# Kernel tuning notes

Measured on AMD Instinct MI355X. Metric: run time of the kernel, lower is better.

The kernel has to match this reference:

```python
import jax, jax.numpy as jnp
import numpy as np

H = W = 256          # render / reference image size (module crops ref to 256x256)
TS = 4               # texture_size in the module
EYE_DIST, ELEV, AZIM = 2.732, 0.0, np.pi / 2  # fixed azimuth (orig: uniform(0,360))
EPS = 1e-8


def _look_at(verts, eye):
    # neural_renderer look_at: at=origin, up=+y
    up = jnp.array([0.0, 1.0, 0.0], dtype=verts.dtype)
    z = -eye / jnp.linalg.norm(eye)
    x = jnp.cross(up, z)
    x = x / jnp.linalg.norm(x)
    y = jnp.cross(z, x)
    R = jnp.stack([x, y, z], axis=0)  # rows = camera axes
    return (verts - eye) @ R.T


def _cross2(u, v):
    return u[..., 0] * v[..., 1] - u[..., 1] * v[..., 0]


def _render(vertices, faces, textures):
    # Orthographic (perspective=False), ambient-only lighting -> color == texture sample.
    eye = jnp.array([EYE_DIST * np.cos(ELEV) * np.sin(AZIM),
                     EYE_DIST * np.sin(ELEV),
                     -EYE_DIST * np.cos(ELEV) * np.cos(AZIM)], dtype=vertices.dtype)
    v = _look_at(vertices[0], eye)            # [V,3] camera space
    fv = v[faces[0]]                          # [F,3,3]
    a, b, c = fv[:, 0, :2], fv[:, 1, :2], fv[:, 2, :2]  # [F,2] screen-space verts
    zf = fv[..., 2]                           # [F,3] per-vertex depth

    # pixel centers in NDC, y flipped (image row 0 = top)
    xs = (jnp.arange(W, dtype=vertices.dtype) + 0.5) / W * 2.0 - 1.0
    ys = 1.0 - (jnp.arange(H, dtype=vertices.dtype) + 0.5) / H * 2.0
    P = jnp.stack(jnp.meshgrid(xs, ys, indexing='xy'), -1).reshape(-1, 2)  # [HW,2]
    Pq = P[:, None, :]                        # [HW,1,2]

    denom = _cross2(b - a, c - a)             # [F] signed 2*area
    w0 = _cross2((c - b)[None], Pq - b[None])  # [HW,F] edge functions
    w1 = _cross2((a - c)[None], Pq - c[None])
    w2 = _cross2((b - a)[None], Pq - a[None])
    s = jnp.sign(denom)[None]
    nondeg = (jnp.abs(denom) > EPS)[None]
    inside = (w0 * s >= 0) & (w1 * s >= 0) & (w2 * s >= 0) & nondeg
    d = jnp.where(jnp.abs(denom) > EPS, denom, 1.0)[None]
    w0, w1, w2 = w0 / d, w1 / d, w2 / d       # normalized barycentrics
    depth = w0 * zf[None, :, 0] + w1 * zf[None, :, 1] + w2 * zf[None, :, 2]  # [HW,F]
    visible = inside & (depth > 0)

    # z-buffer: nearest visible face per pixel
    zbuf = jnp.where(visible, depth, jnp.inf)
    best = jnp.argmin(zbuf, axis=1)           # [HW]
    hit = jnp.take_along_axis(visible, best[:, None], 1)[:, 0]
    bw = jnp.stack([jnp.take_along_axis(wi, best[:, None], 1)[:, 0]
                    for wi in (w0, w1, w2)], axis=-1)  # [HW,3]

    # sample face texture cube [TS,TS,TS] by barycentric coords (nearest)
    ti = jnp.clip(jnp.round(bw * (TS - 1)).astype(jnp.int32), 0, TS - 1)
    color = textures[0][best, ti[:, 0], ti[:, 1], ti[:, 2]]  # [HW,3]
    img = jnp.where(hit[:, None], color, jnp.zeros_like(color)).reshape(H, W, 3)
    return jnp.transpose(img, (2, 0, 1))[None]  # [1,3,H,W]


def setup_inputs() -> dict:
    key = jax.random.key(0)
    k1, k2, k3, k4 = jax.random.split(key, 4)
    V, F = 642, 512
    verts = jax.random.normal(k1, (1, V, 3), jnp.float32)
    verts = verts / (jnp.linalg.norm(verts, axis=-1, keepdims=True) + 1e-6)  # unit sphere
    faces = jax.random.randint(k2, (1, F, 3), 0, V, jnp.int32)
    textures = jax.random.normal(k3, (1, F, TS, TS, TS, 3), jnp.float32)
    image_ref = jax.random.uniform(k4, (1, 3, H, W), jnp.float32)
    return {"vertices": verts, "textures": textures, "image_ref": image_ref, "faces": faces}


def reference(vertices, textures, image_ref, faces):
    image = _render(vertices, faces, jnp.tanh(textures))
    return jnp.sum((image - image_ref) ** 2)
```

## Files before the change

### kernel.cpp

```cpp
#include <hip/hip_runtime.h>
#include <math.h>

#define NFACE 512
#define NVERT 642
#define NPIX  (256 * 256)
#define DXS   (2.0f / 256.0f)

#define EYEX 2.732f
#define EYEZ (-1.6728675276352845e-16f)
#define CC0  (6.123233995736766e-17f)

__global__ __launch_bounds__(256) void render_loss(
    const float* __restrict__ verts,
    const int*   __restrict__ faces,
    const float* __restrict__ tex,
    const float* __restrict__ ref,
    float* __restrict__ out)
{
    __shared__ float  sverts[NVERT * 3];
    __shared__ float4 sf0[NFACE];
    __shared__ float4 sf1[NFACE];
    __shared__ float4 flist[NFACE];
    __shared__ float4 pl0[NFACE];
    __shared__ float4 pl1[NFACE];
    __shared__ float2 pld[NFACE];
    __shared__ unsigned marr[4][256];
    __shared__ int   fcnt, pcnt;
    __shared__ unsigned Mu;
    __shared__ float wsum[4];

    int tid = threadIdx.x;
    if (tid == 0) { fcnt = 0; pcnt = 0; Mu = 0x7f800000u; }

    for (int k = tid; k < NVERT * 3; k += 256) sverts[k] = verts[k];
    __syncthreads();

    int tileX = (blockIdx.x & 15) << 4;
    int tileY = (blockIdx.x >> 4) << 4;
    float xlo = (tileX + 0.5f)  * DXS - 1.0f;
    float xhi = (tileX + 15.5f) * DXS - 1.0f;
    float yhi = 1.0f - (tileY + 0.5f)  * DXS;
    float ylo = 1.0f - (tileY + 15.5f) * DXS;

    float rc[2][9];
    int   rcls[2];
    float rdmn[2];
#pragma unroll
    for (int it = 0; it < 2; ++it) {
        int f = tid + it * 256;
        rcls[it] = 0;
        float vx[3], vy[3], vz[3];
#pragma unroll
        for (int k = 0; k < 3; ++k) {
            int vi = faces[f * 3 + k];
            float px = sverts[vi * 3 + 0];
            float py = sverts[vi * 3 + 1];
            float pz = sverts[vi * 3 + 2];
            float dx = px - EYEX;
            float dz = pz - EYEZ;
            vx[k] = CC0 * dx + dz;
            vy[k] = py;
            vz[k] = -dx + CC0 * dz;
        }
        float ax = vx[0], ay = vy[0];
        float bx = vx[1], by = vy[1];
        float cx = vx[2], cy = vy[2];
        float denom = (bx - ax) * (cy - ay) - (by - ay) * (cx - ax);
        if (fabsf(denom) <= 1e-8f) continue;

        float si = 1.0f / denom;
        float e0x = cx - bx, e0y = cy - by;
        float e1x = ax - cx, e1y = ay - cy;
        float e2x = bx - ax, e2y = by - ay;
        float A0 = e0x * si, B0 = -e0y * si, C0 = (e0y * bx - e0x * by) * si;
        float A1 = e1x * si, B1 = -e1y * si, C1 = (e1y * cx - e1x * cy) * si;
        float A2 = -(A0 + A1), B2 = -(B0 + B1), C2 = 1.0f - C0 - C1;
        float DA = A0 * vz[0] + A1 * vz[1] + A2 * vz[2];
        float DB = B0 * vz[0] + B1 * vz[1] + B2 * vz[2];
        float DC = C0 * vz[0] + C1 * vz[1] + C2 * vz[2];

        sf0[f] = make_float4(A0, B0, C0, A1);
        sf1[f] = make_float4(B1, C1, DA, DB);

        float bxmn = fminf(fminf(ax, bx), cx), bxmx = fmaxf(fmaxf(ax, bx), cx);
        float bymn = fminf(fminf(ay, by), cy), bymx = fmaxf(fmaxf(ay, by), cy);
        if ((bxmn > xhi + 1e-5f) | (bxmx < xlo - 1e-5f) |
            (bymn > yhi + 1e-5f) | (bymx < ylo - 1e-5f)) continue;

        float wmx[3], wmn[3], mg[3];
        float As[3] = {A0, A1, A2}, Bs[3] = {B0, B1, B2}, Cs[3] = {C0, C1, C2};
#pragma unroll
        for (int k = 0; k < 3; ++k) {
            float t1 = As[k] * ylo, t2 = As[k] * yhi;
            float u1 = Bs[k] * xlo, u2 = Bs[k] * xhi;
            wmx[k] = fmaxf(t1, t2) + fmaxf(u1, u2) + Cs[k];
            wmn[k] = fminf(t1, t2) + fminf(u1, u2) + Cs[k];
            mg[k]  = (fabsf(As[k]) + fabsf(Bs[k]) + fabsf(Cs[k])) * 2e-6f;
        }
        if ((wmx[0] < -mg[0]) | (wmx[1] < -mg[1]) | (wmx[2] < -mg[2])) continue;
        bool full = (wmn[0] > mg[0]) & (wmn[1] > mg[1]) & (wmn[2] > mg[2]);

        float t1 = DA * ylo, t2 = DA * yhi;
        float u1 = DB * xlo, u2 = DB * xhi;
        float dmx = fmaxf(t1, t2) + fmaxf(u1, u2) + DC;
        float dmn = fminf(t1, t2) + fminf(u1, u2) + DC;
        float md  = (fabsf(DA) + fabsf(DB) + fabsf(DC)) * 2e-6f + 1e-4f;
        rdmn[it] = dmn - md;
        rcls[it] = full ? 1 : 2;
        rc[it][0] = A0; rc[it][1] = B0; rc[it][2] = C0;
        rc[it][3] = A1; rc[it][4] = B1; rc[it][5] = C1;
        rc[it][6] = DA; rc[it][7] = DB; rc[it][8] = DC;
        if (full) atomicMin(&Mu, __float_as_uint(dmx + md));
    }
    __syncthreads();

    float M = __uint_as_float(Mu);
#pragma unroll
    for (int it = 0; it < 2; ++it) {
        if (rcls[it] == 0 || rdmn[it] > M) continue;
        int f = tid + it * 256;
        float fb = __uint_as_float((unsigned)f);
        if (rcls[it] == 1) {
            int s = atomicAdd(&fcnt, 1);
            flist[s] = make_float4(rc[it][6], rc[it][7], rc[it][8], fb);
        } else {
            int s = atomicAdd(&pcnt, 1);
            pl0[s] = make_float4(rc[it][0], rc[it][1], rc[it][2], rc[it][3]);
            pl1[s] = make_float4(rc[it][4], rc[it][5], rc[it][6], rc[it][7]);
            pld[s] = make_float2(rc[it][8], fb);
        }
    }
    __syncthreads();
    int fc = fcnt, pc = pcnt;

    int lane = tid & 63;
    int w    = tid >> 6;
    int col   = lane & 15;
    int rbase = (lane >> 4) << 2;
    float Px  = (tileX + col + 0.5f) * DXS - 1.0f;
    float Py0 = 1.0f - (tileY + rbase + 0.5f) * DXS;

    unsigned pk0 = 0xFFFFFFFFu, pk1 = 0xFFFFFFFFu;
    unsigned pk2 = 0xFFFFFFFFu, pk3 = 0xFFFFFFFFu;

#pragma unroll 2
    for (int k = w; k < fc; k += 4) {
        float4 r = flist[k];
        float td = fmaf(r.y, Px, r.z);
        float d0 = fmaf(r.x, Py0, td);
        float d1 = fmaf(r.x, Py0 - DXS, td);
        float d2 = fmaf(r.x, Py0 - 2.0f * DXS, td);
        float d3 = fmaf(r.x, Py0 - 3.0f * DXS, td);
        unsigned fb = __float_as_uint(r.w);
        unsigned c0 = (__float_as_uint(d0) & 0xFFFFFE00u) | fb;
        unsigned c1 = (__float_as_uint(d1) & 0xFFFFFE00u) | fb;
        unsigned c2 = (__float_as_uint(d2) & 0xFFFFFE00u) | fb;
        unsigned c3 = (__float_as_uint(d3) & 0xFFFFFE00u) | fb;
        pk0 = pk0 < c0 ? pk0 : c0;
        pk1 = pk1 < c1 ? pk1 : c1;
        pk2 = pk2 < c2 ? pk2 : c2;
        pk3 = pk3 < c3 ? pk3 : c3;
    }

#pragma unroll 2
    for (int k = w; k < pc; k += 4) {
        float4 q0 = pl0[k];
        float4 q1 = pl1[k];
        float2 qd = pld[k];
        float t0 = fmaf(q0.y, Px, q0.z);
        float t1 = fmaf(q1.x, Px, q1.y);
        float td = fmaf(q1.w, Px, qd.x);
        unsigned fb = __float_as_uint(qd.y);
#pragma unroll
        for (int q = 0; q < 4; ++q) {
            float Py = Py0 - (float)q * DXS;
            float w0 = fmaf(q0.x, Py, t0);
            float w1 = fmaf(q0.w, Py, t1);
            float w2 = 1.0f - w0 - w1;
            float dp = fmaf(q1.z, Py, td);
            float mn = fminf(fminf(w0, w1), w2);
            unsigned cd = (__float_as_uint(dp) & 0xFFFFFE00u) | fb;
            cd = (mn >= 0.f) ? cd : 0xFFFFFFFFu;
            if (q == 0) pk0 = pk0 < cd ? pk0 : cd;
            if (q == 1) pk1 = pk1 < cd ? pk1 : cd;
            if (q == 2) pk2 = pk2 < cd ? pk2 : cd;
            if (q == 3) pk3 = pk3 < cd ? pk3 : cd;
        }
    }

    marr[w][(rbase + 0) * 16 + col] = pk0;
    marr[w][(rbase + 1) * 16 + col] = pk1;
    marr[w][(rbase + 2) * 16 + col] = pk2;
    marr[w][(rbase + 3) * 16 + col] = pk3;
    __syncthreads();
    unsigned best = marr[0][tid];
    unsigned m1 = marr[1][tid];
    unsigned m2 = marr[2][tid];
    unsigned m3 = marr[3][tid];
    best = best < m1 ? best : m1;
    best = best < m2 ? best : m2;
    best = best < m3 ? best : m3;

    int i = tileX + (tid & 15);
    int j = tileY + (tid >> 4);
    float Pxe = (i + 0.5f) * DXS - 1.0f;
    float Pye = 1.0f - (j + 0.5f) * DXS;
    int p = j * 256 + i;
    float col0 = 0.f, col1 = 0.f, col2 = 0.f;
    if (best != 0xFFFFFFFFu) {
        int bf = (int)(best & 511u);
        float4 q0 = sf0[bf];
        float4 q1 = sf1[bf];
        float w0 = fmaf(q0.x, Pye, fmaf(q0.y, Pxe, q0.z));
        float w1 = fmaf(q0.w, Pye, fmaf(q1.x, Pxe, q1.y));
        float w2 = 1.0f - w0 - w1;
        int t0 = (int)rintf(w0 * 3.0f); t0 = t0 < 0 ? 0 : (t0 > 3 ? 3 : t0);
        int t1 = (int)rintf(w1 * 3.0f); t1 = t1 < 0 ? 0 : (t1 > 3 ? 3 : t1);
        int t2 = (int)rintf(w2 * 3.0f); t2 = t2 < 0 ? 0 : (t2 > 3 ? 3 : t2);
        const float* tp = tex + ((((bf * 4 + t0) * 4 + t1) * 4 + t2) * 3);
        col0 = tanhf(tp[0]);
        col1 = tanhf(tp[1]);
        col2 = tanhf(tp[2]);
    }
    float r0 = ref[0 * NPIX + p];
    float r1 = ref[1 * NPIX + p];
    float r2 = ref[2 * NPIX + p];
    float e0 = col0 - r0, e1 = col1 - r1, e2 = col2 - r2;
    float loss = e0 * e0 + e1 * e1 + e2 * e2;

    for (int off = 32; off > 0; off >>= 1)
        loss += __shfl_down(loss, off, 64);
    if (lane == 0) wsum[w] = loss;
    __syncthreads();
    if (tid == 0)
        atomicAdd(out, wsum[0] + wsum[1] + wsum[2] + wsum[3]);
}

extern "C" void kernel_launch(void* const* d_in, const int* in_sizes, int n_in,
                              void* d_out, int out_size, void* d_ws, size_t ws_size,
                              hipStream_t stream) {
    const float* verts = (const float*)d_in[0];
    const float* tex   = (const float*)d_in[1];
    const float* ref   = (const float*)d_in[2];
    const int*   faces = (const int*)d_in[3];
    float* out = (float*)d_out;

    hipMemsetAsync(out, 0, sizeof(float), stream);
    render_loss<<<256, 256, 0, stream>>>(verts, faces, tex, ref, out);
}
```

Baseline: 17.47 us.

## Halve tile height, use wave-aggregated list appends and last-block reduction

Tiles shrink from 16x16 to 16x8 pixels, so 512 blocks run instead of 256 and per-tile face lists get shorter. Face-list insertion now uses one ballot-based atomic per wavefront instead of one per thread. The shading step recomputes the chosen face's barycentric coefficients from the vertices rather than storing them in shared memory, which frees LDS. The memset plus per-block float atomic on the output is replaced by per-block partial sums in the workspace and a final reduction by the last block, which removes the memset launch. Risks: face setup is duplicated across twice as many blocks, only half the threads do shading work, and the workspace counter is never reset, relying on wraparound modulo 512.

```diff
diff --git a/kernel.cpp b/kernel.cpp
--- a/kernel.cpp
+++ b/kernel.cpp
@@ -15,32 +15,35 @@
     const int*   __restrict__ faces,
     const float* __restrict__ tex,
     const float* __restrict__ ref,
+    float* __restrict__ bsum,
+    unsigned* __restrict__ cntr,
     float* __restrict__ out)
 {
     __shared__ float  sverts[NVERT * 3];
-    __shared__ float4 sf0[NFACE];
-    __shared__ float4 sf1[NFACE];
     __shared__ float4 flist[NFACE];
     __shared__ float4 pl0[NFACE];
     __shared__ float4 pl1[NFACE];
     __shared__ float2 pld[NFACE];
-    __shared__ unsigned marr[4][256];
+    __shared__ unsigned marr[4][128];
     __shared__ int   fcnt, pcnt;
     __shared__ unsigned Mu;
     __shared__ float wsum[4];
-
-    int tid = threadIdx.x;
-    if (tid == 0) { fcnt = 0; pcnt = 0; Mu = 0x7f800000u; }
+    __shared__ int sfinish;
+
+    int tid  = threadIdx.x;
+    int lane = tid & 63;
+    int w    = tid >> 6;
+    if (tid == 0) { fcnt = 0; pcnt = 0; Mu = 0x7f800000u; sfinish = 0; }
 
     for (int k = tid; k < NVERT * 3; k += 256) sverts[k] = verts[k];
     __syncthreads();
 
     int tileX = (blockIdx.x & 15) << 4;
-    int tileY = (blockIdx.x >> 4) << 4;
+    int tileY = (blockIdx.x >> 4) << 3;
     float xlo = (tileX + 0.5f)  * DXS - 1.0f;
     float xhi = (tileX + 15.5f) * DXS - 1.0f;
-    float yhi = 1.0f - (tileY + 0.5f)  * DXS;
-    float ylo = 1.0f - (tileY + 15.5f) * DXS;
+    float yhi = 1.0f - (tileY + 0.5f) * DXS;
+    float ylo = 1.0f - (tileY + 7.5f) * DXS;
 
     float rc[2][9];
     int   rcls[2];
@@ -71,16 +74,12 @@
         float si = 1.0f / denom;
         float e0x = cx - bx, e0y = cy - by;
         float e1x = ax - cx, e1y = ay - cy;
-        float e2x = bx - ax, e2y = by - ay;
         float A0 = e0x * si, B0 = -e0y * si, C0 = (e0y * bx - e0x * by) * si;
         float A1 = e1x * si, B1 = -e1y * si, C1 = (e1y * cx - e1x * cy) * si;
         float A2 = -(A0 + A1), B2 = -(B0 + B1), C2 = 1.0f - C0 - C1;
         float DA = A0 * vz[0] + A1 * vz[1] + A2 * vz[2];
         float DB = B0 * vz[0] + B1 * vz[1] + B2 * vz[2];
         float DC = C0 * vz[0] + C1 * vz[1] + C2 * vz[2];
-
-        sf0[f] = make_float4(A0, B0, C0, A1);
-        sf1[f] = make_float4(B1, C1, DA, DB);
 
         float bxmn = fminf(fminf(ax, bx), cx), bxmx = fmaxf(fmaxf(ax, bx), cx);
         float bymn = fminf(fminf(ay, by), cy), bymx = fmaxf(fmaxf(ay, by), cy);
@@ -115,16 +114,28 @@
     __syncthreads();
 
     float M = __uint_as_float(Mu);
+    unsigned long long ltm = (1ull << lane) - 1ull;
 #pragma unroll
     for (int it = 0; it < 2; ++it) {
-        if (rcls[it] == 0 || rdmn[it] > M) continue;
-        int f = tid + it * 256;
-        float fb = __uint_as_float((unsigned)f);
-        if (rcls[it] == 1) {
-            int s = atomicAdd(&fcnt, 1);
+        bool alive = (rcls[it] != 0) && (rdmn[it] <= M);
+        bool isf = alive && (rcls[it] == 1);
+        bool isp = alive && (rcls[it] == 2);
+        unsigned long long bf = __ballot(isf);
+        unsigned long long bp = __ballot(isp);
+        int fbase = 0, pbase = 0;
+        if (lane == 0) {
+            if (bf) fbase = atomicAdd(&fcnt, (int)__popcll(bf));
+            if (bp) pbase = atomicAdd(&pcnt, (int)__popcll(bp));
+        }
+        fbase = __shfl(fbase, 0, 64);
+        pbase = __shfl(pbase, 0, 64);
+        float fb = __uint_as_float((unsigned)(tid + it * 256));
+        if (isf) {
+            int s = fbase + (int)__popcll(bf & ltm);
             flist[s] = make_float4(rc[it][6], rc[it][7], rc[it][8], fb);
-        } else {
-            int s = atomicAdd(&pcnt, 1);
+        }
+        if (isp) {
+            int s = pbase + (int)__popcll(bp & ltm);
             pl0[s] = make_float4(rc[it][0], rc[it][1], rc[it][2], rc[it][3]);
             pl1[s] = make_float4(rc[it][4], rc[it][5], rc[it][6], rc[it][7]);
             pld[s] = make_float2(rc[it][8], fb);
@@ -133,36 +144,25 @@
     __syncthreads();
     int fc = fcnt, pc = pcnt;
 
-    int lane = tid & 63;
-    int w    = tid >> 6;
     int col   = lane & 15;
-    int rbase = (lane >> 4) << 2;
+    int rbase = (lane >> 4) << 1;
     float Px  = (tileX + col + 0.5f) * DXS - 1.0f;
     float Py0 = 1.0f - (tileY + rbase + 0.5f) * DXS;
 
     unsigned pk0 = 0xFFFFFFFFu, pk1 = 0xFFFFFFFFu;
-    unsigned pk2 = 0xFFFFFFFFu, pk3 = 0xFFFFFFFFu;
-
-#pragma unroll 2
+
     for (int k = w; k < fc; k += 4) {
         float4 r = flist[k];
         float td = fmaf(r.y, Px, r.z);
         float d0 = fmaf(r.x, Py0, td);
         float d1 = fmaf(r.x, Py0 - DXS, td);
-        float d2 = fmaf(r.x, Py0 - 2.0f * DXS, td);
-        float d3 = fmaf(r.x, Py0 - 3.0f * DXS, td);
         unsigned fb = __float_as_uint(r.w);
         unsigned c0 = (__float_as_uint(d0) & 0xFFFFFE00u) | fb;
         unsigned c1 = (__float_as_uint(d1) & 0xFFFFFE00u) | fb;
-        unsigned c2 = (__float_as_uint(d2) & 0xFFFFFE00u) | fb;
-        unsigned c3 = (__float_as_uint(d3) & 0xFFFFFE00u) | fb;
         pk0 = pk0 < c0 ? pk0 : c0;
         pk1 = pk1 < c1 ? pk1 : c1;
-        pk2 = pk2 < c2 ? pk2 : c2;
-        pk3 = pk3 < c3 ? pk3 : c3;
-    }
-
-#pragma unroll 2
+    }
+
     for (int k = w; k < pc; k += 4) {
         float4 q0 = pl0[k];
         float4 q1 = pl1[k];
@@ -172,7 +172,7 @@
         float td = fmaf(q1.w, Px, qd.x);
         unsigned fb = __float_as_uint(qd.y);
 #pragma unroll
-        for (int q = 0; q < 4; ++q) {
+        for (int q = 0; q < 2; ++q) {
             float Py = Py0 - (float)q * DXS;
             float w0 = fmaf(q0.x, Py, t0);
             float w1 = fmaf(q0.w, Py, t1);
@@ -183,57 +183,90 @@
             cd = (mn >= 0.f) ? cd : 0xFFFFFFFFu;
             if (q == 0) pk0 = pk0 < cd ? pk0 : cd;
             if (q == 1) pk1 = pk1 < cd ? pk1 : cd;
-            if (q == 2) pk2 = pk2 < cd ? pk2 : cd;
-            if (q == 3) pk3 = pk3 < cd ? pk3 : cd;
         }
     }
 
     marr[w][(rbase + 0) * 16 + col] = pk0;
     marr[w][(rbase + 1) * 16 + col] = pk1;
-    marr[w][(rbase + 2) * 16 + col] = pk2;
-    marr[w][(rbase + 3) * 16 + col] = pk3;
-    __syncthreads();
-    unsigned best = marr[0][tid];
-    unsigned m1 = marr[1][tid];
-    unsigned m2 = marr[2][tid];
-    unsigned m3 = marr[3][tid];
-    best = best < m1 ? best : m1;
-    best = best < m2 ? best : m2;
-    best = best < m3 ? best : m3;
-
-    int i = tileX + (tid & 15);
-    int j = tileY + (tid >> 4);
-    float Pxe = (i + 0.5f) * DXS - 1.0f;
-    float Pye = 1.0f - (j + 0.5f) * DXS;
-    int p = j * 256 + i;
-    float col0 = 0.f, col1 = 0.f, col2 = 0.f;
-    if (best != 0xFFFFFFFFu) {
-        int bf = (int)(best & 511u);
-        float4 q0 = sf0[bf];
-        float4 q1 = sf1[bf];
-        float w0 = fmaf(q0.x, Pye, fmaf(q0.y, Pxe, q0.z));
-        float w1 = fmaf(q0.w, Pye, fmaf(q1.x, Pxe, q1.y));
-        float w2 = 1.0f - w0 - w1;
-        int t0 = (int)rintf(w0 * 3.0f); t0 = t0 < 0 ? 0 : (t0 > 3 ? 3 : t0);
-        int t1 = (int)rintf(w1 * 3.0f); t1 = t1 < 0 ? 0 : (t1 > 3 ? 3 : t1);
-        int t2 = (int)rintf(w2 * 3.0f); t2 = t2 < 0 ? 0 : (t2 > 3 ? 3 : t2);
-        const float* tp = tex + ((((bf * 4 + t0) * 4 + t1) * 4 + t2) * 3);
-        col0 = tanhf(tp[0]);
-        col1 = tanhf(tp[1]);
-        col2 = tanhf(tp[2]);
-    }
-    float r0 = ref[0 * NPIX + p];
-    float r1 = ref[1 * NPIX + p];
-    float r2 = ref[2 * NPIX + p];
-    float e0 = col0 - r0, e1 = col1 - r1, e2 = col2 - r2;
-    float loss = e0 * e0 + e1 * e1 + e2 * e2;
+    __syncthreads();
+
+    float loss = 0.f;
+    if (tid < 128) {
+        unsigned best = marr[0][tid];
+#pragma unroll
+        for (int ww = 1; ww < 4; ++ww) {
+            unsigned m = marr[ww][tid];
+            best = best < m ? best : m;
+        }
+        int i = tileX + (tid & 15);
+        int j = tileY + (tid >> 4);
+        float Pxe = (i + 0.5f) * DXS - 1.0f;
+        float Pye = 1.0f - (j + 0.5f) * DXS;
+        int p = j * 256 + i;
+        float col0 = 0.f, col1 = 0.f, col2 = 0.f;
+        if (best != 0xFFFFFFFFu) {
+            int bf = (int)(best & 511u);
+            float vx[3], vy[3];
+#pragma unroll
+            for (int kk = 0; kk < 3; ++kk) {
+                int vi = faces[bf * 3 + kk];
+                float px = sverts[vi * 3 + 0];
+                float py = sverts[vi * 3 + 1];
+                float pz = sverts[vi * 3 + 2];
+                float dx = px - EYEX;
+                float dz = pz - EYEZ;
+                vx[kk] = CC0 * dx + dz;
+                vy[kk] = py;
+            }
+            float ax = vx[0], ay = vy[0];
+            float bx = vx[1], by = vy[1];
+            float cx = vx[2], cy = vy[2];
+            float denom = (bx - ax) * (cy - ay) - (by - ay) * (cx - ax);
+            float si = 1.0f / denom;
+            float e0x = cx - bx, e0y = cy - by;
+            float e1x = ax - cx, e1y = ay - cy;
+            float A0 = e0x * si, B0 = -e0y * si, C0 = (e0y * bx - e0x * by) * si;
+            float A1 = e1x * si, B1 = -e1y * si, C1 = (e1y * cx - e1x * cy) * si;
+            float w0 = fmaf(A0, Pye, fmaf(B0, Pxe, C0));
+            float w1 = fmaf(A1, Pye, fmaf(B1, Pxe, C1));
+            float w2 = 1.0f - w0 - w1;
+            int t0 = (int)rintf(w0 * 3.0f); t0 = t0 < 0 ? 0 : (t0 > 3 ? 3 : t0);
+            int t1 = (int)rintf(w1 * 3.0f); t1 = t1 < 0 ? 0 : (t1 > 3 ? 3 : t1);
+            int t2 = (int)rintf(w2 * 3.0f); t2 = t2 < 0 ? 0 : (t2 > 3 ? 3 : t2);
+            const float* tp = tex + ((((bf * 4 + t0) * 4 + t1) * 4 + t2) * 3);
+            col0 = tanhf(tp[0]);
+            col1 = tanhf(tp[1]);
+            col2 = tanhf(tp[2]);
+        }
+        float r0 = ref[0 * NPIX + p];
+        float r1 = ref[1 * NPIX + p];
+        float r2 = ref[2 * NPIX + p];
+        float e0 = col0 - r0, e1 = col1 - r1, e2 = col2 - r2;
+        loss = e0 * e0 + e1 * e1 + e2 * e2;
+    }
 
     for (int off = 32; off > 0; off >>= 1)
         loss += __shfl_down(loss, off, 64);
     if (lane == 0) wsum[w] = loss;
     __syncthreads();
-    if (tid == 0)
-        atomicAdd(out, wsum[0] + wsum[1] + wsum[2] + wsum[3]);
+
+    if (tid == 0) {
+        bsum[blockIdx.x] = wsum[0] + wsum[1] + wsum[2] + wsum[3];
+        __threadfence();
+        unsigned old = atomicAdd(cntr, 1u);
+        if ((old & 511u) == 511u) sfinish = 1;
+    }
+    __syncthreads();
+    if (sfinish) {
+        __threadfence();
+        float v = atomicAdd(&bsum[tid], 0.0f) + atomicAdd(&bsum[tid + 256], 0.0f);
+        for (int off = 32; off > 0; off >>= 1)
+            v += __shfl_down(v, off, 64);
+        if (lane == 0) wsum[w] = v;
+        __syncthreads();
+        if (tid == 0)
+            out[0] = wsum[0] + wsum[1] + wsum[2] + wsum[3];
+    }
 }
 
 extern "C" void kernel_launch(void* const* d_in, const int* in_sizes, int n_in,
@@ -243,8 +276,9 @@
     const float* tex   = (const float*)d_in[1];
     const float* ref   = (const float*)d_in[2];
     const int*   faces = (const int*)d_in[3];
-    float* out = (float*)d_out;
-
-    hipMemsetAsync(out, 0, sizeof(float), stream);
-    render_loss<<<256, 256, 0, stream>>>(verts, faces, tex, ref, out);
+    float* out  = (float*)d_out;
+    float* bsum = (float*)d_ws;
+    unsigned* cntr = (unsigned*)((float*)d_ws + 512);
+
+    render_loss<<<512, 256, 0, stream>>>(verts, faces, tex, ref, bsum, cntr, out);
 }
```

After: 19.21 us. +9.9%, slower.
